# Kernel tuning notes

Hardware: AMD Instinct MI355X
Metric: run time of the kernel (lower is better)

Reference implementation:

```python
import jax, jax.numpy as jnp
import numpy as np

B, H, S, W, F = 16, 4, 8, 256, 16


def setup_inputs() -> dict:
    key = jax.random.key(0)
    kx, kk = jax.random.split(key)
    x = jax.random.normal(kx, (B, S, W, F), dtype=jnp.float32)
    kernel = jax.random.normal(kk, (H, S, S, W), dtype=jnp.float32)
    return {"x": x, "kernel": kernel}


def reference(x, kernel):
    # kernel: [H, S, S, W]; x: [B, S, W, F]
    Hh, Ss, _, Ww = kernel.shape
    r = jnp.arange(Ww)
    # stacked[h,x,y,j,i] = roll(kernel, shifts=j+1)[i] = kernel[(i-(j+1)) % W]
    idx = (r[None, :] - (r[:, None] + 1)) % Ww          # [W(row=j), W(col=i)]
    stacked = kernel[..., idx]                            # [H,S,S,W,W]
    # torch.tril over last two dims: keep col i <= row j
    tri = (r[None, :] <= r[:, None])                      # [W,W]
    stacked = jnp.where(tri, stacked, jnp.zeros((), dtype=stacked.dtype))
    # masked triangular time-mix contraction
    out = jnp.einsum('hxyji,bxif->bhxyjf', stacked, x)    # [B,H,S,S,W,F]
    base = jnp.arange(1, Ww + 1, dtype=out.dtype).reshape(1, 1, 1, 1, Ww, 1)
    out = out / base
    # transform_x: on diagonal series (x==y) roll time dim by 1, zero first step
    diag_mod = jnp.roll(out, 1, axis=4)
    not_first = (r != 0).reshape(1, 1, 1, 1, Ww, 1)
    diag_mod = diag_mod * not_first.astype(out.dtype)
    eye = jnp.eye(Ss, dtype=bool).reshape(1, 1, Ss, Ss, 1, 1)
    return jnp.where(eye, diag_mod, out)
```

## Files before the change

kernel.cpp:

```cpp
#include <hip/hip_runtime.h>
#include <hip/hip_bf16.h>

typedef short short8 __attribute__((ext_vector_type(8)));
typedef float f32x4 __attribute__((ext_vector_type(4)));

union FragAB { unsigned long long l[2]; int i[4]; short8 v; };

__global__ __launch_bounds__(256, 2)
void k_fused(const float* __restrict__ x,
             const float* __restrict__ kern,
             float* __restrict__ out)
{
    __shared__ __align__(16) ushort Xts[128 * 264];
    __shared__ __align__(8)  ushort wforL[2][4][336];

    const int blk = blockIdx.x;
    const int c  = blk & 15;
    const int nt = (blk >> 4) & 1;
    const int mt = (blk >> 5) & 1;
    const int sx = blk >> 6;
    const int t = threadIdx.x;

    #pragma unroll
    for (int e2 = 0; e2 < 2; ++e2) {
        const int hy = c * 2 + e2;
        const int h = hy >> 3, sy = hy & 7;
        const float* krow = kern + ((h * 8 + sx) * 8 + sy) * 256;
        #pragma unroll
        for (int s = 0; s < 4; ++s) {
            #pragma unroll
            for (int pass = 0; pass < 2; ++pass) {
                int q = t + pass * 256;
                if (q < 336) {
                    int src = q - s;
                    float v = (src >= 0 && src < 256) ? krow[src] : 0.0f;
                    __hip_bfloat16 hv = __float2bfloat16(v);
                    wforL[e2][s][q] = reinterpret_cast<ushort&>(hv);
                }
            }
        }
    }

    {
        const float4* xbase = reinterpret_cast<const float4*>(x);
        const int b0 = nt * 8;
        #pragma unroll
        for (int it = 0; it < 16; ++it) {
            int id = it * 256 + t;
            int fq = id & 3;
            int k2 = (id >> 2) & 127;
            int bl = id >> 9;
            const float4* rowp = xbase + ((size_t)((b0 + bl) * 8 + sx)) * 1024;
            float4 a = rowp[(2 * k2) * 4 + fq];
            float4 cq = rowp[(2 * k2 + 1) * 4 + fq];
            #pragma unroll
            for (int e = 0; e < 4; ++e) {
                float va = (&a.x)[e], vb = (&cq.x)[e];
                __hip_bfloat16 ha = __float2bfloat16(va);
                __hip_bfloat16 hb = __float2bfloat16(vb);
                uint u = (uint)reinterpret_cast<ushort&>(ha) |
                         ((uint)reinterpret_cast<ushort&>(hb) << 16);
                int row = bl * 16 + fq * 4 + e;
                *reinterpret_cast<uint*>(reinterpret_cast<char*>(Xts) + row * 528 + k2 * 4) = u;
            }
        }
    }
    __syncthreads();

    const int lane = t & 63, wid = t >> 6;
    const int wp = wid >> 1, wj = wid & 1;
    const int laneM = lane & 15, laneG = lane >> 4;
    const int wj0 = mt * 128 + wj * 64;
    const int kmax = wj0 + 64;

    const char* XtsB = reinterpret_cast<const char*>(Xts);
    const char* WB = reinterpret_cast<const char*>(wforL);
    const int abyte = (wp * 64 + laneM) * 528 + laneG * 16;

    int bB[2];
    int diagv[2];
    #pragma unroll
    for (int e2 = 0; e2 < 2; ++e2) {
        const int hy = c * 2 + e2;
        const int sy = hy & 7;
        const int diag = (sx == sy) ? 1 : 0;
        diagv[e2] = diag;
        const int w00 = 255 + diag - wj0 - laneM + 8 * laneG;
        const int s = (laneM - diag + 1) & 3;
        bB[e2] = e2 * 2688 + s * 674 + 2 * w00;
    }

    f32x4 acc[2][4][4];
    #pragma unroll
    for (int e2 = 0; e2 < 2; ++e2)
        #pragma unroll
        for (int m = 0; m < 4; ++m)
            #pragma unroll
            for (int n = 0; n < 4; ++n)
                acc[e2][m][n] = (f32x4){0.0f, 0.0f, 0.0f, 0.0f};

    for (int kc = 0; kc < kmax; kc += 32) {
        FragAB af[4];
        #pragma unroll
        for (int m = 0; m < 4; ++m) {
            const int4 raw = *reinterpret_cast<const int4*>(XtsB + abyte + m * 8448 + kc * 2);
            af[m].i[0] = raw.x; af[m].i[1] = raw.y;
            af[m].i[2] = raw.z; af[m].i[3] = raw.w;
        }
        #pragma unroll
        for (int e2 = 0; e2 < 2; ++e2) {
            FragAB bf[4];
            #pragma unroll
            for (int n = 0; n < 4; ++n) {
                const char* p = WB + bB[e2] + kc * 2 - 32 * n;
                bf[n].l[0] = *reinterpret_cast<const unsigned long long*>(p);
                bf[n].l[1] = *reinterpret_cast<const unsigned long long*>(p + 8);
            }
            #pragma unroll
            for (int m = 0; m < 4; ++m)
                #pragma unroll
                for (int n = 0; n < 4; ++n)
                    acc[e2][m][n] = __builtin_amdgcn_mfma_f32_16x16x32_bf16(
                        af[m].v, bf[n].v, acc[e2][m][n], 0, 0, 0);
        }
    }

    #pragma unroll
    for (int e2 = 0; e2 < 2; ++e2) {
        const int hy = c * 2 + e2;
        const int h = hy >> 3, sy = hy & 7;
        const int diag = diagv[e2];
        #pragma unroll
        for (int n = 0; n < 4; ++n) {
            const int j = wj0 + 16 * n + laneM;
            const int denom = j + 1 - diag;
            const float rt = (denom > 0) ? (1.0f / (float)denom) : 0.0f;
            #pragma unroll
            for (int m = 0; m < 4; ++m) {
                const int b_ = nt * 8 + wp * 4 + m;
                float* dst = out + ((((size_t)(b_ * 4 + h) * 8 + sx) * 8 + sy) * 256 + j) * 16
                             + laneG * 4;
                float4 v;
                v.x = acc[e2][m][n][0] * rt;
                v.y = acc[e2][m][n][1] * rt;
                v.z = acc[e2][m][n][2] * rt;
                v.w = acc[e2][m][n][3] * rt;
                *reinterpret_cast<float4*>(dst) = v;
            }
        }
    }
}

extern "C" void kernel_launch(void* const* d_in, const int* in_sizes, int n_in,
                              void* d_out, int out_size, void* d_ws, size_t ws_size,
                              hipStream_t stream) {
    const float* x    = (const float*)d_in[0];
    const float* kern = (const float*)d_in[1];
    float* out = (float*)d_out;

    k_fused<<<512, 256, 0, stream>>>(x, kern, out);
}
```

Baseline: 24.54 us.

## Split accumulation per head-pair and remap block order by mt

Processes the two (h,sy) series one at a time, each with its own 4x4 accumulator set and a store right after its K loop. This halves the live accumulator registers and lets the first half of the stores overlap with the second series' compute. It also puts mt in the top bits of the block index, so blocks with the lighter causal K range (mt=0) are launched first, changing scheduling order. The cost is that the A fragments are now reloaded from LDS once per series instead of being shared.

After: 22.14 us. -9.8%, faster.

```diff
diff --git a/kernel.cpp b/kernel.cpp
--- a/kernel.cpp
+++ b/kernel.cpp
@@ -15,10 +15,12 @@
     __shared__ __align__(8)  ushort wforL[2][4][336];
 
     const int blk = blockIdx.x;
-    const int c  = blk & 15;
-    const int nt = (blk >> 4) & 1;
-    const int mt = (blk >> 5) & 1;
-    const int sx = blk >> 6;
+    const int id = blk & 255;
+    const int c  = id & 15;
+    const int nt = (id >> 4) & 1;
+    const int sx = id >> 5;
+    const int mt = blk >> 8;
+
     const int t = threadIdx.x;
 
     #pragma unroll
@@ -46,10 +48,10 @@
         const int b0 = nt * 8;
         #pragma unroll
         for (int it = 0; it < 16; ++it) {
-            int id = it * 256 + t;
-            int fq = id & 3;
-            int k2 = (id >> 2) & 127;
-            int bl = id >> 9;
+            int id4 = it * 256 + t;
+            int fq = id4 & 3;
+            int k2 = (id4 >> 2) & 127;
+            int bl = id4 >> 9;
             const float4* rowp = xbase + ((size_t)((b0 + bl) * 8 + sx)) * 1024;
             float4 a = rowp[(2 * k2) * 4 + fq];
             float4 cq = rowp[(2 * k2 + 1) * 4 + fq];
@@ -77,42 +79,34 @@
     const char* WB = reinterpret_cast<const char*>(wforL);
     const int abyte = (wp * 64 + laneM) * 528 + laneG * 16;
 
-    int bB[2];
-    int diagv[2];
     #pragma unroll
     for (int e2 = 0; e2 < 2; ++e2) {
         const int hy = c * 2 + e2;
-        const int sy = hy & 7;
+        const int h = hy >> 3, sy = hy & 7;
         const int diag = (sx == sy) ? 1 : 0;
-        diagv[e2] = diag;
         const int w00 = 255 + diag - wj0 - laneM + 8 * laneG;
         const int s = (laneM - diag + 1) & 3;
-        bB[e2] = e2 * 2688 + s * 674 + 2 * w00;
-    }
+        const int bB = e2 * 2688 + s * 674 + 2 * w00;
 
-    f32x4 acc[2][4][4];
-    #pragma unroll
-    for (int e2 = 0; e2 < 2; ++e2)
+        f32x4 acc[4][4];
         #pragma unroll
         for (int m = 0; m < 4; ++m)
             #pragma unroll
             for (int n = 0; n < 4; ++n)
-                acc[e2][m][n] = (f32x4){0.0f, 0.0f, 0.0f, 0.0f};
+                acc[m][n] = (f32x4){0.0f, 0.0f, 0.0f, 0.0f};
 
-    for (int kc = 0; kc < kmax; kc += 32) {
-        FragAB af[4];
-        #pragma unroll
-        for (int m = 0; m < 4; ++m) {
-            const int4 raw = *reinterpret_cast<const int4*>(XtsB + abyte + m * 8448 + kc * 2);
-            af[m].i[0] = raw.x; af[m].i[1] = raw.y;
-            af[m].i[2] = raw.z; af[m].i[3] = raw.w;
-        }
-        #pragma unroll
-        for (int e2 = 0; e2 < 2; ++e2) {
+        for (int kc = 0; kc < kmax; kc += 32) {
+            FragAB af[4];
+            #pragma unroll
+            for (int m = 0; m < 4; ++m) {
+                const int4 raw = *reinterpret_cast<const int4*>(XtsB + abyte + m * 8448 + kc * 2);
+                af[m].i[0] = raw.x; af[m].i[1] = raw.y;
+                af[m].i[2] = raw.z; af[m].i[3] = raw.w;
+            }
             FragAB bf[4];
             #pragma unroll
             for (int n = 0; n < 4; ++n) {
-                const char* p = WB + bB[e2] + kc * 2 - 32 * n;
+                const char* p = WB + bB + kc * 2 - 32 * n;
                 bf[n].l[0] = *reinterpret_cast<const unsigned long long*>(p);
                 bf[n].l[1] = *reinterpret_cast<const unsigned long long*>(p + 8);
             }
@@ -120,16 +114,10 @@
             for (int m = 0; m < 4; ++m)
                 #pragma unroll
                 for (int n = 0; n < 4; ++n)
-                    acc[e2][m][n] = __builtin_amdgcn_mfma_f32_16x16x32_bf16(
-                        af[m].v, bf[n].v, acc[e2][m][n], 0, 0, 0);
+                    acc[m][n] = __builtin_amdgcn_mfma_f32_16x16x32_bf16(
+                        af[m].v, bf[n].v, acc[m][n], 0, 0, 0);
         }
-    }
 
-    #pragma unroll
-    for (int e2 = 0; e2 < 2; ++e2) {
-        const int hy = c * 2 + e2;
-        const int h = hy >> 3, sy = hy & 7;
-        const int diag = diagv[e2];
         #pragma unroll
         for (int n = 0; n < 4; ++n) {
             const int j = wj0 + 16 * n + laneM;
@@ -141,10 +129,10 @@
                 float* dst = out + ((((size_t)(b_ * 4 + h) * 8 + sx) * 8 + sy) * 256 + j) * 16
                              + laneG * 4;
                 float4 v;
-                v.x = acc[e2][m][n][0] * rt;
-                v.y = acc[e2][m][n][1] * rt;
-                v.z = acc[e2][m][n][2] * rt;
-                v.w = acc[e2][m][n][3] * rt;
+                v.x = acc[m][n][0] * rt;
+                v.y = acc[m][n][1] * rt;
+                v.z = acc[m][n][2] * rt;
+                v.w = acc[m][n][3] * rt;
                 *reinterpret_cast<float4*>(dst) = v;
             }
         }
```
